# Optimization experiments

Hardware: AMD Instinct MI355X
Metric: run time of the kernel (lower is better)

## Reference

```python
import jax, jax.numpy as jnp
import numpy as np
import math

H, W = 64, 64
WS = 8            # window_size
KS = 8            # kernel_size (depthwise conv stride=kernel)
D = 512           # d_model
CF = 128          # flow_dModel
IC = D + CF       # 640
HEAD = 8
GH, GW = H // WS, W // WS
G = GH * GW       # windows
EPS = 1e-5


def layernorm(x, g, b):
    m = jnp.mean(x, axis=-1, keepdims=True)
    v = jnp.mean((x - m) ** 2, axis=-1, keepdims=True)
    return (x - m) * jax.lax.rsqrt(v + EPS) * g + b


def depthwise_conv(x_nchw, w, b):
    # w: [C, 1, KS, KS], stride=KS, VALID, groups=C
    y = jax.lax.conv_general_dilated(
        x_nchw, w, window_strides=(KS, KS), padding='VALID',
        feature_group_count=x_nchw.shape[1],
        dimension_numbers=('NCHW', 'OIHW', 'NCHW'))
    return y + b[None, :, None, None]


def setup_inputs() -> dict:
    key = jax.random.key(0)
    ks = jax.random.split(key, 24)
    bt = 8
    s = 0.02
    inp = {
        'x': jax.random.normal(ks[0], (bt, H * W, D), jnp.float32),
        'f': jax.random.normal(ks[1], (bt, H * W, CF), jnp.float32),
        't': 2,
        'Wq': jax.random.normal(ks[2], (IC, D), jnp.float32) * s,
        'bq': jnp.zeros((D,), jnp.float32),
        'Wk': jax.random.normal(ks[3], (IC, D), jnp.float32) * s,
        'bk': jnp.zeros((D,), jnp.float32),
        'Wv': jax.random.normal(ks[4], (D, D), jnp.float32) * s,
        'bv': jnp.zeros((D,), jnp.float32),
        'Wo': jax.random.normal(ks[5], (D, D), jnp.float32) * s,
        'bo': jnp.zeros((D,), jnp.float32),
        'convK_w': jax.random.normal(ks[6], (IC, 1, KS, KS), jnp.float32) * s,
        'convK_b': jnp.zeros((IC,), jnp.float32),
        'convV_w': jax.random.normal(ks[7], (D, 1, KS, KS), jnp.float32) * s,
        'convV_b': jnp.zeros((D,), jnp.float32),
        'qn_g': jnp.ones((IC,), jnp.float32), 'qn_b': jnp.zeros((IC,), jnp.float32),
        'kn_g': jnp.ones((IC,), jnp.float32), 'kn_b': jnp.zeros((IC,), jnp.float32),
        'vn_g': jnp.ones((D,), jnp.float32), 'vn_b': jnp.zeros((D,), jnp.float32),
        'rw_W': jax.random.normal(ks[8], (IC, CF), jnp.float32) * s,
        'rw_b': jnp.zeros((CF,), jnp.float32),
    }
    return inp


def reference(x, f, t, Wq, bq, Wk, bk, Wv, bv, Wo, bo,
              convK_w, convK_b, convV_w, convV_b,
              qn_g, qn_b, kn_g, kn_b, vn_g, vn_b, rw_W, rw_b):
    bt, n, c = x.shape
    hd = c // HEAD
    x4 = x.reshape(bt, H, W, c)            # no padding: H, W multiples of WS
    f4 = f.reshape(bt, H, W, CF)

    xf = jnp.concatenate([x4, f4], axis=-1)                 # [bt,H,W,IC]
    flow_w = jax.nn.sigmoid(xf @ rw_W + rw_b)               # [bt,H,W,CF]
    f4 = f4 * flow_w
    qk = jnp.concatenate([x4, f4], axis=-1)                 # [bt,H,W,IC]

    def windows(a):
        cc = a.shape[-1]
        a = a.reshape(bt, GH, WS, GW, WS, cc).transpose(0, 1, 3, 2, 4, 5)
        return a.reshape(bt, G, WS * WS, cc)

    q = windows(qk)                                          # [bt,G,ws2,IC]

    k_glob = depthwise_conv(qk.transpose(0, 3, 1, 2), convK_w, convK_b)
    k_glob = k_glob.transpose(0, 2, 3, 1).reshape(bt, -1, IC)  # [bt,M,IC]
    M = k_glob.shape[1]
    k_glob = jnp.broadcast_to(k_glob[:, None], (bt, G, M, IC))
    k = jnp.concatenate([q, k_glob], axis=2)                 # [bt,G,ws2+M,IC]

    q = layernorm(q, qn_g, qn_b)
    k = layernorm(k, kn_g, kn_b)

    v_glob = depthwise_conv(x4.transpose(0, 3, 1, 2), convV_w, convV_b)
    v_glob = v_glob.transpose(0, 2, 3, 1).reshape(bt, -1, c)
    v_glob = jnp.broadcast_to(v_glob[:, None], (bt, G, M, c))
    xw = windows(x4)
    v = jnp.concatenate([xw, v_glob], axis=2)                # [bt,G,ws2+M,c]
    v = layernorm(v, vn_g, vn_b)

    query = q @ Wq + bq                                      # [bt,G,ws2,c]
    key = k @ Wk + bk
    value = v @ Wv + bv

    Lk = key.shape[2]
    query = query.reshape(bt, G, WS * WS, HEAD, hd).transpose(0, 1, 3, 2, 4)
    key = key.reshape(bt, G, Lk, HEAD, hd).transpose(0, 1, 3, 2, 4)
    value = value.reshape(bt, G, Lk, HEAD, hd).transpose(0, 1, 3, 2, 4)

    scores = jnp.einsum('bghqd,bghkd->bghqk', query, key) / math.sqrt(hd)
    attn = jax.nn.softmax(scores, axis=-1)
    out = jnp.einsum('bghqk,bghkd->bghqd', attn, value)      # [bt,G,H,ws2,hd]

    out = out.transpose(0, 1, 3, 2, 4).reshape(bt, GH, GW, WS, WS, c)
    out = out.transpose(0, 1, 3, 2, 4, 5).reshape(bt, H, W, c).reshape(bt, n, c)
    return out @ Wo + bo
```

## Files before the change

### kernel.cpp

```cpp
#include <hip/hip_runtime.h>
#include <hip/hip_bf16.h>

typedef __hip_bfloat16 bf16;
typedef __attribute__((ext_vector_type(8))) short bf16x8;
typedef __attribute__((ext_vector_type(8))) unsigned short ushort8;
typedef __attribute__((ext_vector_type(4))) float f32x4;

#define BT 8
#define HH 64
#define WW 64
#define NSP (HH*WW)
#define DD 512
#define CF 128
#define IC 640
#define NG 64
#define NM 64
#define TRI 1536
#define EPS 1e-5f

static __device__ __forceinline__ float b2f(bf16 v) { return __bfloat162float(v); }
static __device__ __forceinline__ bf16 f2b(float v) { return __float2bfloat16(v); }
static __device__ __forceinline__ float u2f(unsigned short u) {
    return __uint_as_float((unsigned)u << 16);
}
static __device__ __forceinline__ unsigned short f2u(float v) {
    bf16 b = __float2bfloat16(v);
    return __builtin_bit_cast(unsigned short, b);
}

__global__ void detect_dtype(const void* __restrict__ x, int* __restrict__ flag) {
    __shared__ int cnt;
    if (threadIdx.x == 0) cnt = 0;
    __syncthreads();
    const unsigned* w = (const unsigned*)x;
    int local = 0;
    for (int i = threadIdx.x; i < 4096; i += 256) {
        float v = __uint_as_float(w[i]);
        float a = fabsf(v);
        if (a > 1e-5f && a < 1e4f) local++;
    }
    atomicAdd(&cnt, local);
    __syncthreads();
    if (threadIdx.x == 0) *flag = (cnt > 2048) ? 1 : 0;
}

#define NW 20
struct WTab {
    const void* src[NW];
    int pre[NW + 1];
};

__global__ void convert_weights(WTab t, const int* __restrict__ flag,
                                bf16* __restrict__ dst, int total) {
    int fp32 = *flag;
    for (int idx = blockIdx.x * blockDim.x + threadIdx.x; idx < total;
         idx += gridDim.x * blockDim.x) {
        int seg = 0;
        #pragma unroll
        for (int i = 0; i < NW; ++i) if (idx >= t.pre[i + 1]) seg = i + 1;
        int local = idx - t.pre[seg];
        bf16 v;
        if (fp32) v = f2b(((const float*)t.src[seg])[local]);
        else      v = ((const bf16*)t.src[seg])[local];
        dst[idx] = v;
    }
}

#define NSEG 7
struct TT {
    int srcoff[NSEG], dstoff[NSEG], R[NSEG], C[NSEG], dstride[NSEG], tpre[NSEG + 1];
};
__global__ void transpose_weights(const bf16* __restrict__ wc, bf16* __restrict__ wt, TT t) {
    __shared__ unsigned short tile[32][33];
    int tb = blockIdx.x;
    int seg = 0;
    while (tb >= t.tpre[seg + 1]) seg++;
    int lt = tb - t.tpre[seg];
    int C = t.C[seg];
    int tpr = C / 32;
    int r0 = (lt / tpr) * 32, c0 = (lt % tpr) * 32;
    int ds = t.dstride[seg];
    const unsigned short* src = (const unsigned short*)(wc + t.srcoff[seg]);
    unsigned short* dst = (unsigned short*)(wt + t.dstoff[seg]);
    int tx = threadIdx.x & 31, ty = threadIdx.x >> 5;
    #pragma unroll
    for (int i = 0; i < 4; ++i)
        tile[ty + i * 8][tx] = src[(long long)(r0 + ty + i * 8) * C + c0 + tx];
    __syncthreads();
    #pragma unroll
    for (int i = 0; i < 4; ++i)
        dst[(long long)(c0 + ty + i * 8) * ds + r0 + tx] = tile[tx][ty + i * 8];
}

__global__ void fold_ln_weights(bf16* __restrict__ WT, int stride,
                                const bf16* __restrict__ g,
                                const bf16* __restrict__ b, const bf16* __restrict__ bias,
                                float* __restrict__ colsum, float* __restrict__ bias2,
                                int K, int Kpad) {
    int n = blockIdx.x;
    bf16* wrow = WT + (long long)n * stride;
    float s1 = 0.f, s2 = 0.f;
    for (int k = threadIdx.x; k < K; k += 256) {
        float w = b2f(wrow[k]);
        float gk = b2f(g[k]);
        wrow[k] = f2b(w * gk);
        s1 += w * gk;
        s2 += w * b2f(b[k]);
    }
    for (int k = K + threadIdx.x; k < Kpad; k += 256) wrow[k] = f2b(0.f);
    __shared__ float r1[256], r2[256];
    r1[threadIdx.x] = s1; r2[threadIdx.x] = s2;
    __syncthreads();
    for (int off = 128; off > 0; off >>= 1) {
        if (threadIdx.x < off) {
            r1[threadIdx.x] += r1[threadIdx.x + off];
            r2[threadIdx.x] += r2[threadIdx.x + off];
        }
        __syncthreads();
    }
    if (threadIdx.x == 0) {
        colsum[n] = r1[0];
        bias2[n]  = b2f(bias[n]) + r2[0];
    }
}

__global__ void assemble_qk_v(const void* __restrict__ xv, const void* __restrict__ fv,
                              const int* __restrict__ flag, bf16* __restrict__ qk,
                              int rows, long long xoff, long long foff) {
    int fp32 = *flag;
    long long total = (long long)rows * 80;
    for (long long i = (long long)blockIdx.x * blockDim.x + threadIdx.x; i < total;
         i += (long long)gridDim.x * blockDim.x) {
        int row = (int)(i / 80);
        int g = (int)(i % 80);
        ushort8 o;
        if (g < 64) {
            long long s = xoff + (long long)row * DD + g * 8;
            if (fp32) {
                const float* xp = (const float*)xv + s;
                #pragma unroll
                for (int e = 0; e < 8; ++e) o[e] = f2u(xp[e]);
            } else {
                o = *(const ushort8*)((const unsigned short*)xv + s);
            }
        } else {
            long long s = foff + (long long)row * CF + (g - 64) * 8;
            if (fp32) {
                const float* fp = (const float*)fv + s;
                #pragma unroll
                for (int e = 0; e < 8; ++e) o[e] = f2u(fp[e]);
            } else {
                o = *(const ushort8*)((const unsigned short*)fv + s);
            }
        }
        *(ushort8*)((unsigned short*)qk + (long long)row * IC + g * 8) = o;
    }
}

__global__ __launch_bounds__(256)
void dwconv_fast(const bf16* __restrict__ qk,
                 const bf16* __restrict__ wkT, const bf16* __restrict__ bk_,
                 const bf16* __restrict__ wvT, const bf16* __restrict__ bv_,
                 bf16* __restrict__ kg, bf16* __restrict__ vg) {
    int bid = blockIdx.x;
    int chunk = bid % 10;
    int bm = bid / 10;
    int b = bm >> 6, m = bm & 63;
    int my = m >> 3, mx = m & 7;
    int tid = threadIdx.x;
    int c8 = tid & 7;
    int pg = tid >> 3;
    int cbase = chunk * 64 + c8 * 8;
    const unsigned short* sb = (const unsigned short*)qk + (long long)b * NSP * IC;
    const unsigned short* wku = (const unsigned short*)wkT;
    const unsigned short* wvu = (const unsigned short*)wvT;
    bool doV = chunk < 8;
    float ak[8] = {0,0,0,0,0,0,0,0}, av[8] = {0,0,0,0,0,0,0,0};
    #pragma unroll
    for (int pp = 0; pp < 2; ++pp) {
        int p = pg + pp * 32;
        int ky = p >> 3, kx = p & 7;
        int pos = (my * 8 + ky) * WW + mx * 8 + kx;
        ushort8 q = *(const ushort8*)&sb[(long long)pos * IC + cbase];
        ushort8 wk8 = *(const ushort8*)&wku[p * IC + cbase];
        #pragma unroll
        for (int e = 0; e < 8; ++e) ak[e] += u2f(q[e]) * u2f(wk8[e]);
        if (doV) {
            ushort8 wv8 = *(const ushort8*)&wvu[p * DD + cbase];
            #pragma unroll
            for (int e = 0; e < 8; ++e) av[e] += u2f(q[e]) * u2f(wv8[e]);
        }
    }
    #pragma unroll
    for (int off = 8; off <= 32; off <<= 1) {
        #pragma unroll
        for (int e = 0; e < 8; ++e) {
            ak[e] += __shfl_xor(ak[e], off, 64);
            av[e] += __shfl_xor(av[e], off, 64);
        }
    }
    __shared__ float lds[2][4][8][8];
    int wave = tid >> 6, lane = tid & 63;
    if (lane < 8) {
        #pragma unroll
        for (int e = 0; e < 8; ++e) {
            lds[0][wave][lane][e] = ak[e];
            lds[1][wave][lane][e] = av[e];
        }
    }
    __syncthreads();
    if (tid < 64) {
        int cc8 = tid >> 3, e = tid & 7;
        int c = chunk * 64 + cc8 * 8 + e;
        float k4 = lds[0][0][cc8][e] + lds[0][1][cc8][e]
                 + lds[0][2][cc8][e] + lds[0][3][cc8][e];
        kg[(long long)bm * IC + c] = f2b(k4 + b2f(bk_[c]));
        if (doV) {
            float v4 = lds[1][0][cc8][e] + lds[1][1][cc8][e]
                     + lds[1][2][cc8][e] + lds[1][3][cc8][e];
            vg[(long long)bm * IC + c] = f2b(v4 + b2f(bv_[c]));
        } else {
            vg[(long long)bm * IC + c] = f2b(0.f);
        }
    }
}

__global__ void stats_fused(const bf16* __restrict__ qk, float* __restrict__ stats_full,
                            float* __restrict__ stats_x, int rows) {
    int gt = blockIdx.x * blockDim.x + threadIdx.x;
    int wid = gt >> 6;
    int lane = gt & 63;
    if (wid >= rows) return;
    const unsigned short* p = (const unsigned short*)qk + (long long)wid * IC;
    ushort8 v = *(const ushort8*)(p + lane * 8);
    float s1 = 0.f, ss1 = 0.f, s2 = 0.f, ss2 = 0.f;
    #pragma unroll
    for (int e = 0; e < 8; ++e) { float f = u2f(v[e]); s1 += f; ss1 += f * f; }
    if (lane < 16) {
        ushort8 v2 = *(const ushort8*)(p + DD + lane * 8);
        #pragma unroll
        for (int e = 0; e < 8; ++e) { float f = u2f(v2[e]); s2 += f; ss2 += f * f; }
    }
    #pragma unroll
    for (int off = 32; off > 0; off >>= 1) {
        s1  += __shfl_down(s1,  off, 64);
        ss1 += __shfl_down(ss1, off, 64);
        s2  += __shfl_down(s2,  off, 64);
        ss2 += __shfl_down(ss2, off, 64);
    }
    if (lane == 0) {
        float m1 = s1 / 512.f;
        float var1 = ss1 / 512.f - m1 * m1;
        stats_x[wid * 2]     = m1;
        stats_x[wid * 2 + 1] = rsqrtf(var1 + EPS);
        float st = s1 + s2, sst = ss1 + ss2;
        float m2 = st / 640.f;
        float var2 = sst / 640.f - m2 * m2;
        stats_full[wid * 2]     = m2;
        stats_full[wid * 2 + 1] = rsqrtf(var2 + EPS);
    }
}

__global__ void stats_kernel(const bf16* __restrict__ X, int lda, float* __restrict__ stats,
                             int rows, int K) {
    int gt = blockIdx.x * blockDim.x + threadIdx.x;
    int wid = gt >> 6;
    int lane = gt & 63;
    if (wid >= rows) return;
    const bf16* p = X + (long long)wid * lda;
    float s = 0.f, ss = 0.f;
    for (int k = lane; k < K; k += 64) {
        float v = b2f(p[k]);
        s += v; ss += v * v;
    }
    #pragma unroll
    for (int off = 32; off > 0; off >>= 1) {
        s  += __shfl_down(s,  off, 64);
        ss += __shfl_down(ss, off, 64);
    }
    if (lane == 0) {
        float m = s / K;
        float var = ss / K - m * m;
        stats[wid * 2]     = m;
        stats[wid * 2 + 1] = rsqrtf(var + EPS);
    }
}

__global__ __launch_bounds__(256)
void gemm_mfma(const bf16* __restrict__ A, int lda,
               const float* __restrict__ statsQK, const float* __restrict__ statsX,
               int nQK,
               const float* __restrict__ colsum, const float* __restrict__ bias2,
               const bf16* __restrict__ Bmat,
               const bf16* __restrict__ bias,
               bf16* __restrict__ C,
               void* __restrict__ Cout, const int* __restrict__ outflag, long long outoff,
               const bf16* __restrict__ A2k, const float* __restrict__ stats2k,
               bf16* __restrict__ C2k,
               const bf16* __restrict__ A2v, const float* __restrict__ stats2v,
               bf16* __restrict__ C2v, int M2,
               int M, int N, int K, int mode) {
    __shared__ unsigned short As[128 * 32];
    __shared__ unsigned short Bs[128 * 32];
    int tid = threadIdx.x;

    int nwgx = gridDim.x;
    int nwg = nwgx * gridDim.y;
    int orig = blockIdx.y * nwgx + blockIdx.x;
    int qq = nwg >> 3, rr = nwg & 7;
    int xcd = orig & 7, idx = orig >> 3;
    int wg = (xcd < rr ? xcd * (qq + 1) : rr * (qq + 1) + (xcd - rr) * qq) + idx;
    int gy = wg / nwgx;
    int gx = wg % nwgx;
    int bn = gx * 128;

    int nby_main = M >> 7;
    const bf16* Ap;
    const float* stp = nullptr;
    bf16* C2 = nullptr;
    int rowbase, mlim, glob, colOff = 0;
    if (gy < nby_main) {
        Ap = A; rowbase = gy * 128; mlim = M; glob = 0;
        if (mode == 2) stp = (bn >= nQK) ? statsX : statsQK;
    } else {
        if (bn < 512) return;
        int isV = bn >= 1024;
        Ap = isV ? A2v : A2k;
        stp = isV ? stats2v : stats2k;
        C2 = isV ? C2v : C2k;
        colOff = isV ? 1024 : 512;
        rowbase = (gy - nby_main) * 128; mlim = M2; glob = 1;
    }

    int wave = tid >> 6, lane = tid & 63;
    int qm = (wave >> 1) * 64;
    int qn = (wave & 1) * 64;
    int lm = lane & 15;
    int kq = (lane >> 4) * 8;
    int sr = lane >> 2;
    int sc = (lane & 3) * 8;

    f32x4 acc[4][4];
    #pragma unroll
    for (int i = 0; i < 4; ++i)
        #pragma unroll
        for (int j = 0; j < 4; ++j)
            acc[i][j] = (f32x4){0.f, 0.f, 0.f, 0.f};

    const unsigned short* Au = (const unsigned short*)Ap;
    const unsigned short* Bu = (const unsigned short*)Bmat;

    for (int k0 = 0; k0 < K; k0 += 32) {
        #pragma unroll
        for (int i = 0; i < 2; ++i) {
            int seg = wave * 2 + i;
            const unsigned short* gp =
                Au + (long long)(rowbase + seg * 16 + sr) * lda + k0 + sc;
            __builtin_amdgcn_global_load_lds(
                (const __attribute__((address_space(1))) void*)gp,
                (__attribute__((address_space(3))) void*)&As[seg * 512], 16, 0, 0);
        }
        #pragma unroll
        for (int i = 0; i < 2; ++i) {
            int seg = wave * 2 + i;
            const unsigned short* gp =
                Bu + (long long)(bn + seg * 16 + sr) * K + k0 + sc;
            __builtin_amdgcn_global_load_lds(
                (const __attribute__((address_space(1))) void*)gp,
                (__attribute__((address_space(3))) void*)&Bs[seg * 512], 16, 0, 0);
        }
        __syncthreads();
        bf16x8 af[4], bfr[4];
        #pragma unroll
        for (int i = 0; i < 4; ++i)
            af[i] = *(const bf16x8*)&As[(qm + i * 16 + lm) * 32 + kq];
        #pragma unroll
        for (int j = 0; j < 4; ++j)
            bfr[j] = *(const bf16x8*)&Bs[(qn + j * 16 + lm) * 32 + kq];
        #pragma unroll
        for (int i = 0; i < 4; ++i)
            #pragma unroll
            for (int j = 0; j < 4; ++j)
                acc[i][j] = __builtin_amdgcn_mfma_f32_16x16x32_bf16(
                    af[i], bfr[j], acc[i][j], 0, 0, 0);
        __syncthreads();
    }

    int rq = (lane >> 4) * 4;
    float cs[4], bb[4];
    #pragma unroll
    for (int j = 0; j < 4; ++j) {
        int col = bn + qn + j * 16 + lm;
        if (mode == 2) { cs[j] = colsum[col]; bb[j] = bias2[col]; }
        else bb[j] = bias ? b2f(bias[col]) : 0.f;
    }
    int ofp = (!glob && outflag) ? *outflag : 0;
    #pragma unroll
    for (int i = 0; i < 4; ++i) {
        #pragma unroll
        for (int r = 0; r < 4; ++r) {
            int row = rowbase + qm + i * 16 + rq + r;
            if (row >= mlim) continue;
            float mean = 0.f, rstd = 0.f;
            if (mode == 2) { mean = stp[row * 2]; rstd = stp[row * 2 + 1]; }
            #pragma unroll
            for (int j = 0; j < 4; ++j) {
                int col = bn + qn + j * 16 + lm;
                float v = acc[i][j][r];
                if (mode == 2) v = rstd * (v - mean * cs[j]) + bb[j];
                else {
                    v += bb[j];
                    if (mode == 3) v = 1.f / (1.f + __expf(-v));
                }
                if (mode == 3) {
                    unsigned short* qp =
                        (unsigned short*)C + (long long)row * IC + DD + col;
                    *qp = f2u(u2f(*qp) * v);
                    continue;
                }
                if (glob) {
                    C2[(long long)row * 512 + (col - colOff)] = f2b(v);
                } else if (outflag) {
                    long long ci = (long long)row * N + col;
                    if (ofp) ((float*)Cout)[outoff + ci] = v;
                    else     ((bf16*)Cout)[outoff + ci] = f2b(v);
                } else {
                    C[(long long)row * N + col] = f2b(v);
                }
            }
        }
    }
}

#define QS_STRIDE 72
#define PS_STRIDE 136
__global__ __launch_bounds__(256)
void attn_kernel(const bf16* __restrict__ qkv,
                 const bf16* __restrict__ key_glob, const bf16* __restrict__ val_glob,
                 bf16* __restrict__ attout) {
    int h = blockIdx.x & 7;
    int g = (blockIdx.x >> 3) & 63;
    int b = blockIdx.x >> 9;
    int gy = g >> 3, gx = g & 7;

    __shared__ unsigned short smem[64 * PS_STRIDE + 64 * PS_STRIDE];
    unsigned short* Qs = smem;
    unsigned short* Ks = smem + 64 * QS_STRIDE;
    unsigned short* Ps = smem;
    unsigned short* Vs = smem + 64 * PS_STRIDE;

    int tid = threadIdx.x;
    const unsigned short* QKV = (const unsigned short*)qkv;
    const unsigned short* KG = (const unsigned short*)key_glob;
    const unsigned short* VG = (const unsigned short*)val_glob;

    #pragma unroll
    for (int it = 0; it < 2; ++it) {
        int i = tid + it * 256;
        int t = i >> 3, dg = (i & 7) * 8;
        int ty = t >> 3, tx = t & 7;
        long long row = (long long)b * NSP + (gy * 8 + ty) * WW + gx * 8 + tx;
        *(ushort8*)&Qs[t * QS_STRIDE + dg] =
            *(const ushort8*)&QKV[row * TRI + h * 64 + dg];
    }
    #pragma unroll
    for (int it = 0; it < 4; ++it) {
        int i = tid + it * 256;
        int t = i >> 3, dg = (i & 7) * 8;
        ushort8 kv;
        if (t < 64) {
            int ty = t >> 3, tx = t & 7;
            long long row = (long long)b * NSP + (gy * 8 + ty) * WW + gx * 8 + tx;
            kv = *(const ushort8*)&QKV[row * TRI + 512 + h * 64 + dg];
        } else {
            long long srow = (long long)b * NM + (t - 64);
            kv = *(const ushort8*)&KG[srow * DD + h * 64 + dg];
        }
        *(ushort8*)&Ks[t * QS_STRIDE + dg] = kv;
    }
    __syncthreads();

    int wave = tid >> 6, lane = tid & 63;
    int m0 = wave * 16;
    int lm = lane & 15;
    int quad = lane >> 4;

    f32x4 sacc[8];
    #pragma unroll
    for (int j = 0; j < 8; ++j) sacc[j] = (f32x4){0.f, 0.f, 0.f, 0.f};
    #pragma unroll
    for (int ks = 0; ks < 2; ++ks) {
        int kq = quad * 8 + ks * 32;
        bf16x8 af = *(const bf16x8*)&Qs[(m0 + lm) * QS_STRIDE + kq];
        #pragma unroll
        for (int j = 0; j < 8; ++j) {
            bf16x8 bfr = *(const bf16x8*)&Ks[(j * 16 + lm) * QS_STRIDE + kq];
            sacc[j] = __builtin_amdgcn_mfma_f32_16x16x32_bf16(af, bfr, sacc[j], 0, 0, 0);
        }
    }
    float pinv[4];
    #pragma unroll
    for (int r = 0; r < 4; ++r) {
        float mx = -1e30f;
        #pragma unroll
        for (int j = 0; j < 8; ++j) {
            sacc[j][r] *= 0.125f;
            mx = fmaxf(mx, sacc[j][r]);
        }
        mx = fmaxf(mx, __shfl_xor(mx, 1, 64));
        mx = fmaxf(mx, __shfl_xor(mx, 2, 64));
        mx = fmaxf(mx, __shfl_xor(mx, 4, 64));
        mx = fmaxf(mx, __shfl_xor(mx, 8, 64));
        float l = 0.f;
        #pragma unroll
        for (int j = 0; j < 8; ++j) {
            float p = __expf(sacc[j][r] - mx);
            sacc[j][r] = p;
            l += p;
        }
        l += __shfl_xor(l, 1, 64);
        l += __shfl_xor(l, 2, 64);
        l += __shfl_xor(l, 4, 64);
        l += __shfl_xor(l, 8, 64);
        pinv[r] = 1.f / l;
    }
    __syncthreads();

    #pragma unroll
    for (int r = 0; r < 4; ++r) {
        int qrow = m0 + quad * 4 + r;
        #pragma unroll
        for (int j = 0; j < 8; ++j)
            Ps[qrow * PS_STRIDE + j * 16 + lm] = f2u(sacc[j][r] * pinv[r]);
    }
    #pragma unroll
    for (int it = 0; it < 4; ++it) {
        int i = tid + it * 256;
        int t = i & 127, dg = (i >> 7) * 8;
        ushort8 v;
        if (t < 64) {
            int ty = t >> 3, tx = t & 7;
            long long row = (long long)b * NSP + (gy * 8 + ty) * WW + gx * 8 + tx;
            v = *(const ushort8*)&QKV[row * TRI + 1024 + h * 64 + dg];
        } else {
            long long srow = (long long)b * NM + (t - 64);
            v = *(const ushort8*)&VG[srow * DD + h * 64 + dg];
        }
        #pragma unroll
        for (int e = 0; e < 8; ++e) Vs[(dg + e) * PS_STRIDE + t] = v[e];
    }
    __syncthreads();

    f32x4 oacc[4];
    #pragma unroll
    for (int j = 0; j < 4; ++j) oacc[j] = (f32x4){0.f, 0.f, 0.f, 0.f};
    #pragma unroll
    for (int ks = 0; ks < 4; ++ks) {
        int kq = quad * 8 + ks * 32;
        bf16x8 af = *(const bf16x8*)&Ps[(m0 + lm) * PS_STRIDE + kq];
        #pragma unroll
        for (int j = 0; j < 4; ++j) {
            bf16x8 bfr = *(const bf16x8*)&Vs[(j * 16 + lm) * PS_STRIDE + kq];
            oacc[j] = __builtin_amdgcn_mfma_f32_16x16x32_bf16(af, bfr, oacc[j], 0, 0, 0);
        }
    }
    #pragma unroll
    for (int r = 0; r < 4; ++r) {
        int qrow = m0 + quad * 4 + r;
        int ty = qrow >> 3, tx = qrow & 7;
        long long orow = (long long)b * NSP + (gy * 8 + ty) * WW + gx * 8 + tx;
        unsigned short* op = (unsigned short*)attout + orow * DD + h * 64;
        #pragma unroll
        for (int j = 0; j < 4; ++j)
            op[j * 16 + lm] = f2u(oacc[j][r]);
    }
}

static inline size_t alg(size_t b) { return (b + 255) & ~(size_t)255; }

extern "C" void kernel_launch(void* const* d_in, const int* in_sizes, int n_in,
                              void* d_out, int out_size, void* d_ws, size_t ws_size,
                              hipStream_t stream) {
    int s = (n_in > 2 && in_sizes[2] == 1) ? 0 : -1;

    const void* xv = d_in[0];
    const void* fv = d_in[1];
    const void* wsrc[NW];
    for (int i = 0; i < NW; ++i) wsrc[i] = d_in[3 + s + i];
    (void)out_size;

    const int wcnt[NW] = {327680, 512, 327680, 512, 262144, 512, 262144, 512,
                          40960, 640, 32768, 512, 640, 640, 640, 640, 512, 512,
                          81920, 128};
    WTab tab;
    int pre = 0;
    for (int i = 0; i < NW; ++i) {
        tab.src[i] = wsrc[i];
        tab.pre[i] = pre;
        pre += wcnt[i];
    }
    tab.pre[NW] = pre;
    const int wtotal = pre;

    char* ws = (char*)d_ws;
    size_t head = 0;
    int* flag = (int*)(ws + head); head += 256;
    bf16* wc = (bf16*)(ws + head); head += alg((size_t)wtotal * 2);
    const int off_qkvW = 0;
    const int off_WoT  = TRI * IC;
    const int off_rwT  = off_WoT + DD * DD;
    const int off_wkT  = off_rwT + CF * IC;
    const int off_wvT  = off_wkT + 64 * IC;
    const int wtpre    = off_wvT + 64 * DD;
    bf16* wt = (bf16*)(ws + head); head += alg((size_t)wtpre * 2);
    float* foldv = (float*)(ws + head); head += alg(2 * TRI * sizeof(float));
    float* cs_qkv = foldv;
    float* b2_qkv = foldv + TRI;

    const bf16* bq     = wc + tab.pre[1];
    const bf16* bk     = wc + tab.pre[3];
    const bf16* bv     = wc + tab.pre[5];
    const bf16* bo     = wc + tab.pre[7];
    const bf16* convKb = wc + tab.pre[9];
    const bf16* convVb = wc + tab.pre[11];
    const bf16* qn_g   = wc + tab.pre[12];
    const bf16* qn_b   = wc + tab.pre[13];
    const bf16* kn_g   = wc + tab.pre[14];
    const bf16* kn_b   = wc + tab.pre[15];
    const bf16* vn_g   = wc + tab.pre[16];
    const bf16* vn_b   = wc + tab.pre[17];
    const bf16* rw_b   = wc + tab.pre[19];
    bf16* qkvW = wt + off_qkvW;
    bf16* WoT  = wt + off_WoT;
    bf16* rwT  = wt + off_rwT;
    bf16* wkT  = wt + off_wkT;
    bf16* wvT  = wt + off_wvT;

    size_t avail = ws_size > head ? ws_size - head : 0;
    auto need = [&](int bc) -> size_t {
        size_t rows = (size_t)bc * NSP;
        size_t gm = (size_t)bc * NM, gmp = gm + 64;
        return alg(rows * IC * 2) + alg(rows * TRI * 2)
             + 2 * alg(gmp * IC * 2) + 2 * alg(gm * DD * 2)
             + 2 * alg(rows * 8) + 2 * alg(gmp * 8);
    };
    int nb = BT;
    while (nb > 1 && need(nb) > avail) nb--;

    detect_dtype<<<1, 256, 0, stream>>>(xv, flag);
    convert_weights<<<(wtotal + 255) / 256, 256, 0, stream>>>(tab, flag, wc, wtotal);
    {
        TT tt;
        const int srcsel[NSEG] = {0, 2, 4, 6, 18, 8, 10};
        const int Rr[NSEG]     = {IC, IC, DD, DD, IC, IC, DD};
        const int Cc[NSEG]     = {DD, DD, DD, DD, CF, 64, 64};
        const int dof[NSEG]    = {0, DD * IC, 2 * DD * IC, off_WoT, off_rwT,
                                  off_wkT, off_wvT};
        const int dstr[NSEG]   = {IC, IC, IC, DD, IC, IC, DD};
        int tp = 0;
        for (int i = 0; i < NSEG; ++i) {
            tt.srcoff[i] = tab.pre[srcsel[i]];
            tt.dstoff[i] = dof[i];
            tt.R[i] = Rr[i];
            tt.C[i] = Cc[i];
            tt.dstride[i] = dstr[i];
            tt.tpre[i] = tp;
            tp += (Rr[i] / 32) * (Cc[i] / 32);
        }
        tt.tpre[NSEG] = tp;
        transpose_weights<<<tp, 256, 0, stream>>>(wc, wt, tt);
    }
    fold_ln_weights<<<DD, 256, 0, stream>>>(qkvW,              IC, qn_g, qn_b, bq,
                                            cs_qkv,       b2_qkv,       IC, IC);
    fold_ln_weights<<<DD, 256, 0, stream>>>(qkvW + DD * IC,    IC, kn_g, kn_b, bk,
                                            cs_qkv + 512, b2_qkv + 512, IC, IC);
    fold_ln_weights<<<DD, 256, 0, stream>>>(qkvW + 2 * DD * IC, IC, vn_g, vn_b, bv,
                                            cs_qkv + 1024, b2_qkv + 1024, DD, IC);

    for (int b0 = 0; b0 < BT; b0 += nb) {
        int bc = BT - b0 < nb ? BT - b0 : nb;
        int rows = bc * NSP;
        int gm = bc * NM;
        int gyg = (gm + 127) / 128;

        size_t off = head;
        auto alloc = [&](size_t bytes) -> void* {
            void* p = ws + off; off += alg(bytes); return p;
        };
        size_t gmp = (size_t)gm + 64;
        bf16* qk        = (bf16*)alloc((size_t)rows * IC * 2);
        bf16* qkv       = (bf16*)alloc((size_t)rows * TRI * 2);
        bf16* kg        = (bf16*)alloc(gmp * IC * 2);
        bf16* vg        = (bf16*)alloc(gmp * IC * 2);
        bf16* key_glob  = (bf16*)alloc((size_t)gm * DD * 2);
        bf16* val_glob  = (bf16*)alloc((size_t)gm * DD * 2);
        float* stats_qk = (float*)alloc((size_t)rows * 8);
        float* stats_x  = (float*)alloc((size_t)rows * 8);
        float* stats_kg = (float*)alloc(gmp * 8);
        float* stats_vg = (float*)alloc(gmp * 8);
        bf16* attout    = qk;

        {
            long long total = (long long)rows * 80;
            int blocks = (int)((total + 255) / 256);
            assemble_qk_v<<<blocks, 256, 0, stream>>>(
                xv, fv, flag, qk, rows,
                (long long)b0 * NSP * DD, (long long)b0 * NSP * CF);
        }
        gemm_mfma<<<dim3(CF / 128, rows / 128), 256, 0, stream>>>(
            qk, IC, nullptr, nullptr, 0, nullptr, nullptr, rwT, rw_b, qk,
            nullptr, nullptr, 0,
            nullptr, nullptr, nullptr, nullptr, nullptr, nullptr, 0,
            rows, CF, IC, 3);
        dwconv_fast<<<bc * NM * 10, 256, 0, stream>>>(
            qk, wkT, convKb, wvT, convVb, kg, vg);
        stats_fused<<<rows / 4, 256, 0, stream>>>(qk, stats_qk, stats_x, rows);
        stats_kernel<<<(gm * 64 + 255) / 256, 256, 0, stream>>>(kg, IC, stats_kg, gm, IC);
        stats_kernel<<<(gm * 64 + 255) / 256, 256, 0, stream>>>(vg, IC, stats_vg, gm, DD);
        gemm_mfma<<<dim3(TRI / 128, rows / 128 + gyg), 256, 0, stream>>>(
            qk, IC, stats_qk, stats_x, 1024, cs_qkv, b2_qkv, qkvW, nullptr, qkv,
            nullptr, nullptr, 0,
            kg, stats_kg, key_glob, vg, stats_vg, val_glob, gm,
            rows, TRI, IC, 2);
        attn_kernel<<<bc * NG * 8, 256, 0, stream>>>(qkv, key_glob, val_glob, attout);
        gemm_mfma<<<dim3(DD / 128, rows / 128), 256, 0, stream>>>(
            attout, DD, nullptr, nullptr, 0, nullptr, nullptr, WoT, bo, nullptr,
            d_out, flag, (long long)b0 * NSP * DD,
            nullptr, nullptr, nullptr, nullptr, nullptr, nullptr, 0,
            rows, DD, DD, 0);
    }
}
```

Before: 500.4 us.

## Triple-buffer GEMM LDS tiles with prefetch two k-steps ahead

Result: no change. 493.5 us (-1.4%).

```diff
diff --git a/kernel.cpp b/kernel.cpp
--- a/kernel.cpp
+++ b/kernel.cpp
@@ -300,8 +300,8 @@
                const bf16* __restrict__ A2v, const float* __restrict__ stats2v,
                bf16* __restrict__ C2v, int M2,
                int M, int N, int K, int mode) {
-    __shared__ unsigned short As[128 * 32];
-    __shared__ unsigned short Bs[128 * 32];
+    __shared__ unsigned short As[3][128 * 32];
+    __shared__ unsigned short Bs[3][128 * 32];
     int tid = threadIdx.x;
 
     int nwgx = gridDim.x;
@@ -350,7 +350,7 @@
     const unsigned short* Au = (const unsigned short*)Ap;
     const unsigned short* Bu = (const unsigned short*)Bmat;
 
-    for (int k0 = 0; k0 < K; k0 += 32) {
+    auto STAGE = [&](int buf, int k0) {
         #pragma unroll
         for (int i = 0; i < 2; ++i) {
             int seg = wave * 2 + i;
@@ -358,7 +358,7 @@
                 Au + (long long)(rowbase + seg * 16 + sr) * lda + k0 + sc;
             __builtin_amdgcn_global_load_lds(
                 (const __attribute__((address_space(1))) void*)gp,
-                (__attribute__((address_space(3))) void*)&As[seg * 512], 16, 0, 0);
+                (__attribute__((address_space(3))) void*)&As[buf][seg * 512], 16, 0, 0);
         }
         #pragma unroll
         for (int i = 0; i < 2; ++i) {
@@ -367,23 +367,42 @@
                 Bu + (long long)(bn + seg * 16 + sr) * K + k0 + sc;
             __builtin_amdgcn_global_load_lds(
                 (const __attribute__((address_space(1))) void*)gp,
-                (__attribute__((address_space(3))) void*)&Bs[seg * 512], 16, 0, 0);
-        }
-        __syncthreads();
+                (__attribute__((address_space(3))) void*)&Bs[buf][seg * 512], 16, 0, 0);
+        }
+    };
+    auto COMPUTE = [&](int buf) {
         bf16x8 af[4], bfr[4];
         #pragma unroll
         for (int i = 0; i < 4; ++i)
-            af[i] = *(const bf16x8*)&As[(qm + i * 16 + lm) * 32 + kq];
+            af[i] = *(const bf16x8*)&As[buf][(qm + i * 16 + lm) * 32 + kq];
         #pragma unroll
         for (int j = 0; j < 4; ++j)
-            bfr[j] = *(const bf16x8*)&Bs[(qn + j * 16 + lm) * 32 + kq];
+            bfr[j] = *(const bf16x8*)&Bs[buf][(qn + j * 16 + lm) * 32 + kq];
+        __builtin_amdgcn_s_setprio(1);
         #pragma unroll
         for (int i = 0; i < 4; ++i)
             #pragma unroll
             for (int j = 0; j < 4; ++j)
                 acc[i][j] = __builtin_amdgcn_mfma_f32_16x16x32_bf16(
                     af[i], bfr[j], acc[i][j], 0, 0, 0);
-        __syncthreads();
+        __builtin_amdgcn_s_setprio(0);
+    };
+
+    int nt = K >> 5;
+    STAGE(0, 0);
+    STAGE(1, 32);
+    asm volatile("s_waitcnt vmcnt(4)" ::: "memory");
+    __builtin_amdgcn_s_barrier();
+    for (int t = 0; t < nt; ++t) {
+        int cur = t % 3;
+        if (t + 2 < nt) STAGE((t + 2) % 3, (t + 2) << 5);
+        COMPUTE(cur);
+        if (t + 2 < nt) {
+            asm volatile("s_waitcnt vmcnt(4)" ::: "memory");
+        } else if (t + 1 < nt) {
+            asm volatile("s_waitcnt vmcnt(0)" ::: "memory");
+        }
+        __builtin_amdgcn_s_barrier();
     }
 
     int rq = (lane >> 4) * 4;
@@ -639,7 +658,7 @@
     size_t avail = ws_size > head ? ws_size - head : 0;
     auto need = [&](int bc) -> size_t {
         size_t rows = (size_t)bc * NSP;
-        size_t gm = (size_t)bc * NM, gmp = gm + 64;
+        size_t gm = (size_t)bc * NM, gmp = gm + 128;
         return alg(rows * IC * 2) + alg(rows * TRI * 2)
              + 2 * alg(gmp * IC * 2) + 2 * alg(gm * DD * 2)
              + 2 * alg(rows * 8) + 2 * alg(gmp * 8);
@@ -687,7 +706,7 @@
         auto alloc = [&](size_t bytes) -> void* {
             void* p = ws + off; off += alg(bytes); return p;
         };
-        size_t gmp = (size_t)gm + 64;
+        size_t gmp = (size_t)gm + 128;
         bf16* qk        = (bf16*)alloc((size_t)rows * IC * 2);
         bf16* qkv       = (bf16*)alloc((size_t)rows * TRI * 2);
         bf16* kg        = (bf16*)alloc(gmp * IC * 2);
```
